# Performance work log

Measured on AMD Instinct MI355X. Metric: run time of the kernel, lower is better.

The kernel has to match this reference:

```python
import jax, jax.numpy as jnp
import numpy as np

N = 100000        # nodes
E = 1600000       # edges (avg degree 16)
IN, HID, OUT = 128, 128, 40
K = 3             # Chebyshev order
NUM_HID = 5       # hidden ChebConv layers between first and last


def setup_inputs() -> dict:
    key = jax.random.key(0)
    ks = jax.random.split(key, 8)
    s = 0.05
    return dict(
        features=jax.random.normal(ks[0], (N, IN), jnp.float32),
        src=jax.random.randint(ks[1], (E,), 0, N),
        dst=jax.random.randint(ks[2], (E,), 0, N),
        W0=jax.random.normal(ks[3], (K * IN, HID), jnp.float32) * s,
        b0=jnp.zeros((HID,), jnp.float32),
        Wh=jax.random.normal(ks[4], (NUM_HID, K * HID, HID), jnp.float32) * s,
        bh=jnp.zeros((NUM_HID, HID), jnp.float32),
        Wl=jax.random.normal(ks[5], (K * HID, OUT), jnp.float32) * s,
        bl=jnp.zeros((OUT,), jnp.float32),
    )


def _cheb_conv(X, src, dst, dinv, W, b):
    """One DGL ChebConv with lambda_max=2 (re_norm=1): relu(cat(X_0..X_{K-1}) @ W + b)."""
    def spmm(Y):  # A_hat @ Y = D^-1/2 A D^-1/2 Y via gather/segment-sum
        msg = (Y * dinv)[src]                                  # [E, d]
        return jax.ops.segment_sum(msg, dst, num_segments=N) * dinv

    X0 = X
    bases = [X0]
    X1 = -spmm(X0)                       # X_1 = -A_hat X  (re_norm - 1 == 0)
    bases.append(X1)
    for _ in range(2, K):
        X2 = -2.0 * spmm(X1) - X0        # X_t = -2 A_hat X_{t-1} - X_{t-2}
        bases.append(X2)
        X0, X1 = X1, X2
    Xt = jnp.concatenate(bases, axis=1)  # [N, K*d]
    return jax.nn.relu(Xt @ W + b)


def reference(features, src, dst, W0, b0, Wh, bh, Wl, bl):
    # symmetric normalization from in-degrees (clamped at 1), as in DGL ChebConv
    deg = jax.ops.segment_sum(jnp.ones((E,), jnp.float32), dst, num_segments=N)
    dinv = jnp.clip(deg, 1.0, None) ** -0.5
    dinv = dinv[:, None]                 # [N, 1]

    h = _cheb_conv(features, src, dst, dinv, W0, b0)
    for i in range(NUM_HID):             # dropout is identity in eval mode
        h = _cheb_conv(h, src, dst, dinv, Wh[i], bh[i])
    return _cheb_conv(h, src, dst, dinv, Wl, bl)
```

## Files before the change

### kernel.cpp

```cpp
#include <hip/hip_runtime.h>
#include <hip/hip_bf16.h>


#define NN 100000
#define EE 1600000
#define FF 128
#define NBK 1563
#define EPB 4096
#define CAP 3072

typedef __attribute__((ext_vector_type(8))) short short8_t;
typedef __attribute__((ext_vector_type(8))) _Float16 half8_t;
typedef __attribute__((ext_vector_type(4))) _Float16 half4_t;
typedef __attribute__((ext_vector_type(4))) float floatx4;
typedef __attribute__((ext_vector_type(4))) float accfrag;


__global__ __launch_bounds__(256) void bhist_kernel(const int* __restrict__ dst,
                                                    int* __restrict__ bcnt) {
    __shared__ int lh[NBK];
    int tid = threadIdx.x;
    for (int j = tid; j < NBK; j += 256) lh[j] = 0;
    __syncthreads();
    int e0 = blockIdx.x * EPB;
#pragma unroll
    for (int k = 0; k < EPB / 256; ++k) {
        int i = e0 + k * 256 + tid;
        if (i < EE) atomicAdd(&lh[dst[i] >> 6], 1);
    }
    __syncthreads();
    for (int j = tid; j < NBK; j += 256)
        if (lh[j] > 0) atomicAdd(&bcnt[j], lh[j]);
}

__global__ __launch_bounds__(256) void scan_p1_kernel(const int* __restrict__ cnt,
                                                      int* __restrict__ bsum, int n) {
    __shared__ int red[8];
    int i = blockIdx.x * 256 + threadIdx.x;
    int v = (i < n) ? cnt[i] : 0;
    for (int off = 32; off > 0; off >>= 1) v += __shfl_down(v, off, 64);
    int wv = threadIdx.x >> 6;
    if ((threadIdx.x & 63) == 0) red[wv] = v;
    __syncthreads();
    if (threadIdx.x == 0) bsum[blockIdx.x] = red[0] + red[1] + red[2] + red[3];
}

__global__ __launch_bounds__(1024) void scan_p2_kernel(int* __restrict__ bsum, int nb) {
    __shared__ int s[1024];
    int tid = threadIdx.x;
    int v = (tid < nb) ? bsum[tid] : 0;
    s[tid] = v;
    __syncthreads();
    for (int off = 1; off < 1024; off <<= 1) {
        int u = (tid >= off) ? s[tid - off] : 0;
        __syncthreads();
        s[tid] += u;
        __syncthreads();
    }
    if (tid < nb) bsum[tid] = s[tid] - v;
}

__global__ __launch_bounds__(256) void scan_p3_kernel(const int* __restrict__ cnt,
                                                      const int* __restrict__ bsum,
                                                      int* __restrict__ out_ptr, int n) {
    __shared__ int s[256];
    int tid = threadIdx.x;
    int i = blockIdx.x * 256 + tid;
    int v = (i < n) ? cnt[i] : 0;
    s[tid] = v;
    __syncthreads();
    for (int off = 1; off < 256; off <<= 1) {
        int u = (tid >= off) ? s[tid - off] : 0;
        __syncthreads();
        s[tid] += u;
        __syncthreads();
    }
    if (i < n) {
        int excl = bsum[blockIdx.x] + s[tid] - v;
        out_ptr[i] = excl;
        if (i == n - 1) out_ptr[n] = excl + v;
    }
}

__global__ __launch_bounds__(256) void bscatter_kernel(
    const int* __restrict__ src, const int* __restrict__ dst,
    const int* __restrict__ bptr, int* __restrict__ bfill, int* __restrict__ ebuf) {
    __shared__ int lh[NBK];
    __shared__ int lbase[NBK];
    int tid = threadIdx.x;
    for (int j = tid; j < NBK; j += 256) lh[j] = 0;
    __syncthreads();
    int e0 = blockIdx.x * EPB;
#pragma unroll
    for (int k = 0; k < EPB / 256; ++k) {
        int i = e0 + k * 256 + tid;
        if (i < EE) atomicAdd(&lh[dst[i] >> 6], 1);
    }
    __syncthreads();
    for (int j = tid; j < NBK; j += 256)
        if (lh[j] > 0) lbase[j] = atomicAdd(&bfill[j], lh[j]);
    __syncthreads();
    for (int j = tid; j < NBK; j += 256) lh[j] = 0;
    __syncthreads();
#pragma unroll
    for (int k = 0; k < EPB / 256; ++k) {
        int i = e0 + k * 256 + tid;
        if (i < EE) {
            int d = dst[i];
            int b = d >> 6;
            int off = atomicAdd(&lh[b], 1);
            ebuf[bptr[b] + lbase[b] + off] = (src[i] << 6) | (d & 63);
        }
    }
}

__global__ __launch_bounds__(256) void csr_build_kernel(
    const int* __restrict__ ebuf, const int* __restrict__ bptr,
    int* __restrict__ rowptr, int* __restrict__ colsrc,
    float* __restrict__ dinv, float* __restrict__ dinv2, float* __restrict__ sdeg) {
    __shared__ int pk[CAP];
    __shared__ int ob[CAP];
    __shared__ int cnt[64];
    __shared__ int sexcl[64];
    __shared__ int fill[64];

    int tid = threadIdx.x;
    int b = blockIdx.x;
    int start = bptr[b];
    int cb = bptr[b + 1] - start;
    if (cb > CAP) cb = CAP;

    if (tid < 64) { cnt[tid] = 0; fill[tid] = 0; }
    __syncthreads();

    for (int i = tid; i < cb; i += 256) {
        int v = ebuf[start + i];
        pk[i] = v;
        atomicAdd(&cnt[v & 63], 1);
    }
    __syncthreads();

    if (tid < 64) {
        int v = cnt[tid];
        int inc = v;
        for (int off = 1; off < 64; off <<= 1) {
            int u = __shfl_up(inc, off, 64);
            if (tid >= off) inc += u;
        }
        int excl = inc - v;
        sexcl[tid] = excl;
        int gnode = b * 64 + tid;
        if (gnode < NN) {
            rowptr[gnode] = start + excl;
            int d = v < 1 ? 1 : v;
            float fd = (float)d;
            dinv[gnode]  = 1.0f / sqrtf(fd);
            dinv2[gnode] = 1.0f / fd;
            sdeg[gnode]  = sqrtf(fd);
        }
    }
    if (b == 0 && tid == 0) rowptr[NN] = EE;
    __syncthreads();

    for (int i = tid; i < cb; i += 256) {
        int v = pk[i];
        int d = v & 63;
        int off = atomicAdd(&fill[d], 1);
        ob[sexcl[d] + off] = v >> 6;
    }
    __syncthreads();

    for (int i = tid; i < cb; i += 256) colsrc[start + i] = ob[i];
}


__global__ __launch_bounds__(256) void wprep_kernel(
    const float* __restrict__ W0, const float* __restrict__ Wh, const float* __restrict__ Wl,
    _Float16* __restrict__ Wh16)
{
    int idx = blockIdx.x * 256 + threadIdx.x;
    const int PER = 128 * 384;
    if (idx >= 7 * PER) return;
    int layer = idx / PER;
    int rem = idx - layer * PER;
    int ncol = rem / 384;
    int k = rem - ncol * 384;
    const float* W; int outc;
    if (layer == 0)      { W = W0; outc = 128; }
    else if (layer < 6)  { W = Wh + (size_t)(layer - 1) * 384 * 128; outc = 128; }
    else                 { W = Wl; outc = 40; }
    float v = (ncol < outc) ? W[(size_t)k * outc + ncol] : 0.f;
    Wh16[idx] = (_Float16)v;
}


__global__ __launch_bounds__(256) void fcvt_kernel(const float* __restrict__ in,
                                                   const float* __restrict__ dinv,
                                                   _Float16* __restrict__ out, int total4) {
    int i = blockIdx.x * 256 + threadIdx.x;
    if (i >= total4) return;
    int node = i >> 5;
    float dv = dinv[node];
    floatx4 v = *(const floatx4*)&in[i * 4];
    half4_t r = { (_Float16)(dv * v.x), (_Float16)(dv * v.y),
                  (_Float16)(dv * v.z), (_Float16)(dv * v.w) };
    *(half4_t*)&out[i * 4] = r;
}


__global__ __launch_bounds__(256) void spmm_h_kernel(
    _Float16* __restrict__ out, const _Float16* __restrict__ Xin,
    const _Float16* __restrict__ Xo, const float* __restrict__ dinv2,
    const int* __restrict__ rp, const int* __restrict__ cs,
    float alpha, float beta, int n)
{
    int slot = threadIdx.x >> 4;
    int lane = threadIdx.x & 15;
    int node = blockIdx.x * 16 + slot;
    if (node >= n) return;
    const half8_t* X8 = (const half8_t*)Xin;
    float acc[8] = { 0.f, 0.f, 0.f, 0.f, 0.f, 0.f, 0.f, 0.f };
    int s = rp[node], e = rp[node + 1];
    int i = s;
    for (; i + 8 <= e; i += 8) {
        int idx[8];
#pragma unroll
        for (int u = 0; u < 8; ++u) idx[u] = cs[i + u];
        half8_t x[8];
#pragma unroll
        for (int u = 0; u < 8; ++u) x[u] = X8[(size_t)idx[u] * 16 + lane];
#pragma unroll
        for (int u = 0; u < 8; ++u)
#pragma unroll
            for (int j = 0; j < 8; ++j) acc[j] += (float)x[u][j];
    }
    for (; i < e; ++i) {
        int sidx = cs[i];
        half8_t x = X8[(size_t)sidx * 16 + lane];
#pragma unroll
        for (int j = 0; j < 8; ++j) acc[j] += (float)x[j];
    }
    float sc = alpha * dinv2[node];
    half8_t r;
    if (beta != 0.f) {
        half8_t o = ((const half8_t*)Xo)[(size_t)node * 16 + lane];
#pragma unroll
        for (int j = 0; j < 8; ++j) r[j] = (_Float16)(sc * acc[j] + beta * (float)o[j]);
    } else {
#pragma unroll
        for (int j = 0; j < 8; ++j) r[j] = (_Float16)(sc * acc[j]);
    }
    ((half8_t*)out)[(size_t)node * 16 + lane] = r;
}


template <int OUTC, int NT, bool HOUT>
__global__ __launch_bounds__(256, 4) void gemm_f16_kernel(
    void* __restrict__ outp, const _Float16* __restrict__ X0,
    const _Float16* __restrict__ X1, const _Float16* __restrict__ X2,
    const _Float16* __restrict__ Wh16, const float* __restrict__ bias,
    const float* __restrict__ sdeg, const float* __restrict__ dinv, int n)
{
    __shared__ _Float16 Ws[NT * 16][136];

    int tid = threadIdx.x;
    int lane = tid & 63;
    int wave = tid >> 6;
    int m15 = lane & 15;
    int quad = lane >> 4;
    int row0 = blockIdx.x * 128 + wave * 32;

    accfrag acc[2][NT];
#pragma unroll
    for (int mi = 0; mi < 2; ++mi)
#pragma unroll
        for (int nj = 0; nj < NT; ++nj) acc[mi][nj] = (accfrag){0.f, 0.f, 0.f, 0.f};

    int r0 = row0 + m15;
    int r1 = r0 + 16;
    size_t ro0 = (size_t)((r0 < n) ? r0 : 0) * 16;
    size_t ro1 = (size_t)((r1 < n) ? r1 : 0) * 16;

    const _Float16* srcs[3] = { X0, X1, X2 };

    for (int sb = 0; sb < 3; ++sb) {
        {
            const int VEC = NT * 256;
#pragma unroll
            for (int v0 = 0; v0 < VEC; v0 += 256) {
                int v = v0 + tid;
                int row = v >> 4;
                int c8 = (v & 15) * 8;
                *(half8_t*)&Ws[row][c8] =
                    *(const half8_t*)(Wh16 + (size_t)row * 384 + sb * 128 + c8);
            }
        }
        __syncthreads();

        const half8_t* Xp8 = (const half8_t*)srcs[sb];
#pragma unroll
        for (int kk = 0; kk < 4; ++kk) {
            int k0 = kk * 32 + quad * 8;
            half8_t a0 = Xp8[ro0 + kk * 4 + quad];
            half8_t a1 = Xp8[ro1 + kk * 4 + quad];
#pragma unroll
            for (int nj = 0; nj < NT; ++nj) {
                half8_t bfr = *(const half8_t*)&Ws[nj * 16 + m15][k0];
                acc[0][nj] = __builtin_amdgcn_mfma_f32_16x16x32_f16(a0, bfr, acc[0][nj], 0, 0, 0);
                acc[1][nj] = __builtin_amdgcn_mfma_f32_16x16x32_f16(a1, bfr, acc[1][nj], 0, 0, 0);
            }
        }
        __syncthreads();
    }

    float rs[2][4];
#pragma unroll
    for (int mi = 0; mi < 2; ++mi)
#pragma unroll
        for (int reg = 0; reg < 4; ++reg) {
            int gr = row0 + mi * 16 + quad * 4 + reg;
            int cg = (gr < n) ? gr : 0;
            rs[mi][reg] = HOUT ? dinv[cg] : sdeg[cg];
        }
#pragma unroll
    for (int nj = 0; nj < NT; ++nj) {
        int col = nj * 16 + m15;
        float bv = (col < OUTC) ? bias[col] : 0.f;
#pragma unroll
        for (int mi = 0; mi < 2; ++mi) {
#pragma unroll
            for (int reg = 0; reg < 4; ++reg) {
                int gr = row0 + mi * 16 + quad * 4 + reg;
                if (gr < n && col < OUTC) {
                    if (HOUT) {
                        float v = acc[mi][nj][reg] + rs[mi][reg] * bv;
                        v = v > 0.f ? v : 0.f;
                        ((_Float16*)outp)[(size_t)gr * OUTC + col] = (_Float16)v;
                    } else {
                        float v = rs[mi][reg] * acc[mi][nj][reg] + bv;
                        v = v > 0.f ? v : 0.f;
                        ((float*)outp)[(size_t)gr * OUTC + col] = v;
                    }
                }
            }
        }
    }
}


extern "C" void kernel_launch(void* const* d_in, const int* in_sizes, int n_in,
                              void* d_out, int out_size, void* d_ws, size_t ws_size,
                              hipStream_t stream) {
    const float* features = (const float*)d_in[0];
    const int*   src      = (const int*)d_in[1];
    const int*   dst      = (const int*)d_in[2];
    const float* W0       = (const float*)d_in[3];
    const float* b0       = (const float*)d_in[4];
    const float* Wh       = (const float*)d_in[5];
    const float* bh       = (const float*)d_in[6];
    const float* Wl       = (const float*)d_in[7];
    const float* bl       = (const float*)d_in[8];
    float* out = (float*)d_out;

    const int N = NN, E = EE;
    const int WTOT = 7 * 128 * 384;
    const int EB = (E + EPB - 1) / EPB;
    const int NB2 = (NBK + 255) / 256;

    char* ws = (char*)d_ws;
    size_t off = 0;
    auto alloc = [&](size_t bytes) -> void* {
        void* p = ws + off;
        off += (bytes + 511) & ~(size_t)511;
        return p;
    };
    int*      bcnt   = (int*)alloc((size_t)NBK * 4);
    int*      bfill  = (int*)alloc((size_t)NBK * 4);
    int*      bptr   = (int*)alloc((size_t)(NBK + 1) * 4);
    int*      bsum   = (int*)alloc((size_t)NB2 * 4);
    int*      rowptr = (int*)alloc((size_t)(N + 1) * 4);
    int*      ebuf   = (int*)alloc((size_t)E * 4);
    int*      colsrc = (int*)alloc((size_t)E * 4);
    float*    dinv   = (float*)alloc((size_t)N * 4);
    float*    dinv2  = (float*)alloc((size_t)N * 4);
    float*    sdeg   = (float*)alloc((size_t)N * 4);
    _Float16* Wh16   = (_Float16*)alloc((size_t)WTOT * 2);
    _Float16* XA     = (_Float16*)alloc((size_t)N * FF * 2);
    _Float16* XB     = (_Float16*)alloc((size_t)N * FF * 2);
    _Float16* B1     = (_Float16*)alloc((size_t)N * FF * 2);
    _Float16* B2     = (_Float16*)alloc((size_t)N * FF * 2);

    hipMemsetAsync(bcnt, 0, (size_t)NBK * 4, stream);
    hipMemsetAsync(bfill, 0, (size_t)NBK * 4, stream);
    bhist_kernel<<<EB, 256, 0, stream>>>(dst, bcnt);
    wprep_kernel<<<(WTOT + 255) / 256, 256, 0, stream>>>(W0, Wh, Wl, Wh16);
    scan_p1_kernel<<<NB2, 256, 0, stream>>>(bcnt, bsum, NBK);
    scan_p2_kernel<<<1, 1024, 0, stream>>>(bsum, NB2);
    scan_p3_kernel<<<NB2, 256, 0, stream>>>(bcnt, bsum, bptr, NBK);
    bscatter_kernel<<<EB, 256, 0, stream>>>(src, dst, bptr, bfill, ebuf);
    csr_build_kernel<<<NBK, 256, 0, stream>>>(ebuf, bptr, rowptr, colsrc, dinv, dinv2, sdeg);
    fcvt_kernel<<<(N * FF / 4 + 255) / 256, 256, 0, stream>>>(features, dinv, XA, N * FF / 4);

    const _Float16* cur = XA;
    _Float16* nxt = XB;
    int spmm_grid = (N + 15) / 16;
    int gemm_grid = (N + 127) / 128;

    for (int layer = 0; layer < 7; ++layer) {
        const float* b;
        bool last = (layer == 6);
        if (layer == 0)      { b = b0; }
        else if (layer < 6)  { b = bh + (layer - 1) * 128; }
        else                 { b = bl; }
        const _Float16* wl16 = Wh16 + (size_t)layer * 128 * 384;

        spmm_h_kernel<<<spmm_grid, 256, 0, stream>>>(B1, cur, cur, dinv2, rowptr, colsrc, -1.f, 0.f, N);
        spmm_h_kernel<<<spmm_grid, 256, 0, stream>>>(B2, B1, cur, dinv2, rowptr, colsrc, -2.f, -1.f, N);

        if (!last)
            gemm_f16_kernel<128, 8, true><<<gemm_grid, 256, 0, stream>>>(
                (void*)nxt, cur, B1, B2, wl16, b, sdeg, dinv, N);
        else
            gemm_f16_kernel<40, 3, false><<<gemm_grid, 256, 0, stream>>>(
                (void*)out, cur, B1, B2, wl16, b, sdeg, dinv, N);

        if (layer < 6) {
            const _Float16* newcur = nxt;
            nxt = (_Float16*)((nxt == XB) ? XA : XB);
            cur = newcur;
        }
    }
}
```

Baseline: 1.297 ms.

## Store node features in 16-column channel-blocked layout for cache-resident SpMM gathers

Result: slower. 2.029 ms (+56.5%).

```diff
diff --git a/kernel.cpp b/kernel.cpp
--- a/kernel.cpp
+++ b/kernel.cpp
@@ -8,6 +8,10 @@
 #define NBK 1563
 #define EPB 4096
 #define CAP 3072
+
+#define NCH 8
+#define CHW 16
+#define CH8 2
 
 typedef __attribute__((ext_vector_type(8))) short short8_t;
 typedef __attribute__((ext_vector_type(8))) _Float16 half8_t;
@@ -200,57 +204,82 @@
     int i = blockIdx.x * 256 + threadIdx.x;
     if (i >= total4) return;
     int node = i >> 5;
+    int q = i & 31;
     float dv = dinv[node];
     floatx4 v = *(const floatx4*)&in[i * 4];
     half4_t r = { (_Float16)(dv * v.x), (_Float16)(dv * v.y),
                   (_Float16)(dv * v.z), (_Float16)(dv * v.w) };
-    *(half4_t*)&out[i * 4] = r;
-}
-
-
-__global__ __launch_bounds__(256) void spmm_h_kernel(
+    int f = q * 4;
+    int ch = f >> 4;
+    int off = f & 15;
+    *(half4_t*)&out[(size_t)ch * ((size_t)NN * CHW) + (size_t)node * CHW + off] = r;
+}
+
+
+__global__ __launch_bounds__(256) void spmm_c_kernel(
     _Float16* __restrict__ out, const _Float16* __restrict__ Xin,
     const _Float16* __restrict__ Xo, const float* __restrict__ dinv2,
     const int* __restrict__ rp, const int* __restrict__ cs,
     float alpha, float beta, int n)
 {
-    int slot = threadIdx.x >> 4;
-    int lane = threadIdx.x & 15;
-    int node = blockIdx.x * 16 + slot;
+    int b = blockIdx.x;
+    int ch = b & 7;
+    int nb = b >> 3;
+    int slot = threadIdx.x >> 1;
+    int lane = threadIdx.x & 1;
+    int node = nb * 128 + slot;
     if (node >= n) return;
-    const half8_t* X8 = (const half8_t*)Xin;
+
+    const size_t cbase = (size_t)ch * ((size_t)NN * CH8);
+    const half8_t* X8c = (const half8_t*)Xin + cbase;
+
     float acc[8] = { 0.f, 0.f, 0.f, 0.f, 0.f, 0.f, 0.f, 0.f };
     int s = rp[node], e = rp[node + 1];
     int i = s;
     for (; i + 8 <= e; i += 8) {
         int idx[8];
 #pragma unroll
-        for (int u = 0; u < 8; ++u) idx[u] = cs[i + u];
+        for (int u = 0; u < 8; ++u) idx[u] = __builtin_nontemporal_load(cs + i + u);
         half8_t x[8];
 #pragma unroll
-        for (int u = 0; u < 8; ++u) x[u] = X8[(size_t)idx[u] * 16 + lane];
+        for (int u = 0; u < 8; ++u) x[u] = X8c[(size_t)idx[u] * CH8 + lane];
 #pragma unroll
         for (int u = 0; u < 8; ++u)
 #pragma unroll
             for (int j = 0; j < 8; ++j) acc[j] += (float)x[u][j];
     }
+    if (i + 4 <= e) {
+        int idx[4];
+#pragma unroll
+        for (int u = 0; u < 4; ++u) idx[u] = __builtin_nontemporal_load(cs + i + u);
+        half8_t x[4];
+#pragma unroll
+        for (int u = 0; u < 4; ++u) x[u] = X8c[(size_t)idx[u] * CH8 + lane];
+#pragma unroll
+        for (int u = 0; u < 4; ++u)
+#pragma unroll
+            for (int j = 0; j < 8; ++j) acc[j] += (float)x[u][j];
+        i += 4;
+    }
     for (; i < e; ++i) {
-        int sidx = cs[i];
-        half8_t x = X8[(size_t)sidx * 16 + lane];
+        int sidx = __builtin_nontemporal_load(cs + i);
+        half8_t x = X8c[(size_t)sidx * CH8 + lane];
 #pragma unroll
         for (int j = 0; j < 8; ++j) acc[j] += (float)x[j];
     }
+
     float sc = alpha * dinv2[node];
     half8_t r;
     if (beta != 0.f) {
-        half8_t o = ((const half8_t*)Xo)[(size_t)node * 16 + lane];
+        half8_t o = __builtin_nontemporal_load(
+            (const half8_t*)Xo + cbase + (size_t)node * CH8 + lane);
 #pragma unroll
         for (int j = 0; j < 8; ++j) r[j] = (_Float16)(sc * acc[j] + beta * (float)o[j]);
     } else {
 #pragma unroll
         for (int j = 0; j < 8; ++j) r[j] = (_Float16)(sc * acc[j]);
     }
-    ((half8_t*)out)[(size_t)node * 16 + lane] = r;
+    ((half8_t*)out)[cbase + (size_t)node * CH8 + lane] = r;
 }
 
 
@@ -278,8 +307,8 @@
 
     int r0 = row0 + m15;
     int r1 = r0 + 16;
-    size_t ro0 = (size_t)((r0 < n) ? r0 : 0) * 16;
-    size_t ro1 = (size_t)((r1 < n) ? r1 : 0) * 16;
+    size_t rb0 = (size_t)((r0 < n) ? r0 : 0) * CH8;
+    size_t rb1 = (size_t)((r1 < n) ? r1 : 0) * CH8;
 
     const _Float16* srcs[3] = { X0, X1, X2 };
 
@@ -301,8 +330,10 @@
 #pragma unroll
         for (int kk = 0; kk < 4; ++kk) {
             int k0 = kk * 32 + quad * 8;
-            half8_t a0 = Xp8[ro0 + kk * 4 + quad];
-            half8_t a1 = Xp8[ro1 + kk * 4 + quad];
+            int f = kk * 4 + quad;
+            size_t cb = (size_t)(f >> 1) * ((size_t)NN * CH8) + (size_t)(f & 1);
+            half8_t a0 = Xp8[cb + rb0];
+            half8_t a1 = Xp8[cb + rb1];
 #pragma unroll
             for (int nj = 0; nj < NT; ++nj) {
                 half8_t bfr = *(const half8_t*)&Ws[nj * 16 + m15][k0];
@@ -335,7 +366,8 @@
                     if (HOUT) {
                         float v = acc[mi][nj][reg] + rs[mi][reg] * bv;
                         v = v > 0.f ? v : 0.f;
-                        ((_Float16*)outp)[(size_t)gr * OUTC + col] = (_Float16)v;
+                        ((_Float16*)outp)[(size_t)nj * ((size_t)NN * CHW) +
+                                          (size_t)gr * CHW + m15] = (_Float16)v;
                     } else {
                         float v = rs[mi][reg] * acc[mi][nj][reg] + bv;
                         v = v > 0.f ? v : 0.f;
@@ -403,7 +435,7 @@
 
     const _Float16* cur = XA;
     _Float16* nxt = XB;
-    int spmm_grid = (N + 15) / 16;
+    int spmm_grid = NCH * ((N + 127) / 128);
     int gemm_grid = (N + 127) / 128;
 
     for (int layer = 0; layer < 7; ++layer) {
@@ -414,8 +446,8 @@
         else                 { b = bl; }
         const _Float16* wl16 = Wh16 + (size_t)layer * 128 * 384;
 
-        spmm_h_kernel<<<spmm_grid, 256, 0, stream>>>(B1, cur, cur, dinv2, rowptr, colsrc, -1.f, 0.f, N);
-        spmm_h_kernel<<<spmm_grid, 256, 0, stream>>>(B2, B1, cur, dinv2, rowptr, colsrc, -2.f, -1.f, N);
+        spmm_c_kernel<<<spmm_grid, 256, 0, stream>>>(B1, cur, cur, dinv2, rowptr, colsrc, -1.f, 0.f, N);
+        spmm_c_kernel<<<spmm_grid, 256, 0, stream>>>(B2, B1, cur, dinv2, rowptr, colsrc, -2.f, -1.f, N);
 
         if (!last)
             gemm_f16_kernel<128, 8, true><<<gemm_grid, 256, 0, stream>>>(
```
